# Kernel tuning notes

Hardware: AMD Instinct MI355X
Metric: run time of the kernel (lower is better)

The kernel has to match this reference:

```python
import jax, jax.numpy as jnp
import numpy as np

N, E = 20000, 320000
CS, CV = 64, 32          # scalar / vector multiplicities of node (= node_pre) irreps
AS_, AV, H = 16, 8, 4    # attn irreps scalar/vector muls, num_heads
NB = 16                  # num_basis
SQRT3 = 1.7320508075688772
SQRT2 = 1.4142135623730951
EPS = 1e-5

# dtp weight layout: [ss(CS), sv(CS), vs(CV), vv0(CV), vv1(CV)] -> numel = 2*CS+3*CV = 224

def _cg_tp(s, v, y0, y1, w_ss, w_sv, w_vs, w_vv0, w_vv1):
    """Depthwise CG tensor product for l<=1.
    s:(E,CS) v:(E,CV,3) y0:(E,) y1:(E,3); weights (E,C) or (C,).
    out scalars (E, CS+CV): 0e x 0e -> 0e, 1o x 1o -> 0e (dot/sqrt3)
    out vectors (E, CS+2*CV, 3): 0e x 1o -> 1o, 1o x 0e -> 1o, 1o x 1o -> 1o (cross/sqrt2)
    """
    out_s = jnp.concatenate([
        w_ss * s * y0[:, None],
        w_vv0 * (jnp.einsum('eci,ei->ec', v, y1) / SQRT3)], axis=-1)
    out_v = jnp.concatenate([
        (w_sv * s)[:, :, None] * y1[:, None, :],
        (w_vs * jnp.ones_like(v[..., 0]))[..., None] * v * y0[:, None, None],
        (w_vv1 * jnp.ones_like(v[..., 0]))[..., None] * (jnp.cross(v, y1[:, None, :]) / SQRT2)], axis=1)
    return out_s, out_v


def _equiv_layernorm(s, v, gamma_s, beta_s, gamma_v):
    mu = jnp.mean(s, axis=-1, keepdims=True)
    var = jnp.var(s, axis=-1, keepdims=True)
    s_n = (s - mu) * jax.lax.rsqrt(var + EPS) * gamma_s + beta_s
    rms = jnp.sqrt(jnp.mean(jnp.sum(v * v, axis=-1), axis=-1, keepdims=True) + EPS)
    v_n = v / rms[..., None] * gamma_v[None, :, None]
    return s_n, v_n


def setup_inputs() -> dict:
    key = jax.random.key(0)
    ks = jax.random.split(key, 26)
    def rn(k, shape, fan):
        return jax.random.normal(k, shape, jnp.float32) / np.sqrt(fan)
    D1S, D1V = CS + CV, CS + 2 * CV          # 96, 128 (dtp output muls)
    WN = 2 * CS + 3 * CV                     # 224 dtp weight numel
    inp = {
        'node': jax.random.normal(ks[0], (N, CS + 3 * CV), jnp.float32),
        'edge_index': jax.random.randint(ks[1], (2, E), 0, N, jnp.int64 if jax.config.jax_enable_x64 else jnp.int32),
        'rbf': jax.random.uniform(ks[2], (E, NB), jnp.float32),
        'rsh': jax.random.normal(ks[3], (E, 4), jnp.float32),
        'gamma_s': jnp.ones((CS,), jnp.float32),
        'beta_s': jnp.zeros((CS,), jnp.float32),
        'gamma_v': jnp.ones((CV,), jnp.float32),
        'Ws_src': rn(ks[4], (CS, CS), CS), 'Wv_src': rn(ks[5], (CV, CV), CV),
        'Ws_dst': rn(ks[6], (CS, CS), CS), 'Wv_dst': rn(ks[7], (CV, CV), CV),
        'W_rbf': rn(ks[8], (NB, WN), NB),
        'W_alpha': rn(ks[9], (D1S, H * AS_), D1S),
        'alpha_dot': rn(ks[10], (1, H, AS_), AS_),
        'Ws_val': rn(ks[11], (D1S, CS), D1S), 'Wv_val': rn(ks[12], (D1V, CV), D1V),
        'Wg': rn(ks[13], (CS, CV), CS),
        'w2_ss': rn(ks[14], (CS,), 1), 'w2_sv': rn(ks[15], (CS,), 1),
        'w2_vs': rn(ks[16], (CV,), 1), 'w2_vv0': rn(ks[17], (CV,), 1), 'w2_vv1': rn(ks[18], (CV,), 1),
        'Ws_vlin': rn(ks[19], (D1S, H * AS_), D1S), 'Wv_vlin': rn(ks[20], (D1V, H * AV), D1V),
        'Wps': rn(ks[21], (H * AS_, CS), H * AS_), 'Wpv': rn(ks[22], (H * AV, CV), H * AV),
    }
    return inp


def reference(node, rbf, rsh, gamma_s, beta_s, gamma_v, Ws_src, Wv_src, Ws_dst, Wv_dst,
              W_rbf, W_alpha, alpha_dot, Ws_val, Wv_val, Wg,
              w2_ss, w2_sv, w2_vs, w2_vv0, w2_vv1, Ws_vlin, Wv_vlin, Wps, Wpv, edge_index):
    n = node.shape[0]
    e = rsh.shape[0]
    s = node[:, :CS]
    v = node[:, CS:].reshape(n, CV, 3)
    # equivariant layer norm
    s_n, v_n = _equiv_layernorm(s, v, gamma_s, beta_s, gamma_v)
    # merge_src / merge_dst (irrep-wise o3.Linear)
    src, dst = edge_index[0], edge_index[1]
    msg_s = (s_n @ Ws_src)[src] + (s_n @ Ws_dst)[dst]                       # (E,CS)
    msg_v = jnp.einsum('ncx,cd->ndx', v_n, Wv_src)[src] + \
            jnp.einsum('ncx,cd->ndx', v_n, Wv_dst)[dst]                     # (E,CV,3)
    y0, y1 = rsh[:, 0], rsh[:, 1:4]
    # dtp1: per-edge weighted CG coupling, weights from rbf
    w1 = rbf @ W_rbf                                                        # (E,224)
    m1_s, m1_v = _cg_tp(msg_s, msg_v, y0, y1,
                        w1[:, :CS], w1[:, CS:2*CS], w1[:, 2*CS:2*CS+CV],
                        w1[:, 2*CS+CV:2*CS+2*CV], w1[:, 2*CS+2*CV:])        # (E,96) (E,128,3)
    # attention logits
    a = (m1_s @ W_alpha).reshape(e, H, AS_)
    a = jnp.where(a > 0, a, 0.2 * a)                                        # LeakyReLU(0.2)
    a = jnp.sum(a * alpha_dot, axis=-1, keepdims=True)                      # (E,H,1)
    # softmax over incoming edges of each destination node
    amax = jax.ops.segment_max(a, dst, num_segments=n)
    amax = jnp.where(jnp.isfinite(amax), amax, 0.0)
    ex = jnp.exp(a - amax[dst])
    den = jax.ops.segment_sum(ex, dst, num_segments=n)
    alpha = ex / (den[dst] + 1e-16)                                         # (E,H,1)
    # value path
    val_s = m1_s @ Ws_val                                                   # (E,CS)
    val_v = jnp.einsum('ecx,cd->edx', m1_v, Wv_val)                         # (E,CV,3)
    # gate: sigmoid on scalars, vectors gated by sigmoid of learned scalar gates
    val_v = val_v * jax.nn.sigmoid(val_s @ Wg)[..., None]
    val_s = jax.nn.sigmoid(val_s)
    # dtp2: shared internal weights
    m2_s, m2_v = _cg_tp(val_s, val_v, y0, y1, w2_ss, w2_sv, w2_vs, w2_vv0, w2_vv1)
    # value_lin -> (attn_irreps * num_heads), head-major layout
    hs = (m2_s @ Ws_vlin).reshape(e, H, AS_)
    hv = jnp.einsum('ecx,cd->edx', m2_v, Wv_vlin).reshape(e, H, AV, 3)
    h = jnp.concatenate([hs, hv.reshape(e, H, AV * 3)], axis=-1)            # (E,H,40)
    # attend + scatter-add to destination nodes
    agg = jax.ops.segment_sum(alpha * h, dst, num_segments=n)               # (N,H,40)
    agg_s = agg[:, :, :AS_].reshape(n, H * AS_)                             # (N,64)
    agg_v = agg[:, :, AS_:].reshape(n, H * AV, 3)                           # (N,32,3)
    out = node + jnp.concatenate([
        agg_s @ Wps,
        jnp.einsum('ncx,cd->ndx', agg_v, Wpv).reshape(n, CV * 3)], axis=-1)
    return out
```

## Files before the change

kernel.cpp:

```cpp
#include <hip/hip_runtime.h>
#include <hip/hip_bf16.h>
#include <cstddef>

typedef __hip_bfloat16 bf16;
typedef __bf16 bfv8 __attribute__((ext_vector_type(8)));
typedef __bf16 bfv4 __attribute__((ext_vector_type(4)));
typedef __bf16 bfv2 __attribute__((ext_vector_type(2)));
typedef float f4 __attribute__((ext_vector_type(4)));

#define EPSN 1e-5f
#define SQRT3_INV 0.57735026918962576f
#define SQRT2_INV 0.70710678118654752f

__device__ __forceinline__ float b2f(bf16 x) { return __bfloat162float(x); }

template<int BF> __device__ __forceinline__ float ldf(const void* p, size_t i) {
    if (BF) return __bfloat162float(((const bf16*)p)[i]);
    return ((const float*)p)[i];
}
__device__ __forceinline__ float ldr(const void* p, size_t i, int bfm) {
    return bfm ? __bfloat162float(((const bf16*)p)[i]) : ((const float*)p)[i];
}
template<int BF> __device__ __forceinline__ void stf(void* p, size_t i, float v) {
    if (BF) ((bf16*)p)[i] = __float2bfloat16(v);
    else    ((float*)p)[i] = v;
}

__device__ __forceinline__ float wave_sum64(float x) {
    #pragma unroll
    for (int m = 1; m < 64; m <<= 1) x += __shfl_xor(x, m, 64);
    return x;
}

__device__ __forceinline__ f4 mf(bfv8 a, bfv8 b, f4 c) {
    return __builtin_amdgcn_mfma_f32_16x16x32_bf16(a, b, c, 0, 0, 0);
}

__global__ __launch_bounds__(256) void k_sniff(const void* node, const void* eidx, int* flags)
{
    int t = threadIdx.x;
    __shared__ int cnt;
    __shared__ unsigned orr;
    if (t == 0) { cnt = 0; orr = 0u; }
    __syncthreads();
    unsigned w  = ((const unsigned*)node)[t];
    unsigned lo = w & 0xFFFFu;
    int e_lo = (int)((lo >> 7) & 0xFF);
    if (e_lo >= 96 && e_lo <= 140) atomicAdd(&cnt, 1);
    unsigned odd = ((const unsigned*)eidx)[2 * t + 1];
    atomicOr(&orr, odd);
    __syncthreads();
    if (t == 0) {
        flags[0] = (cnt >= 128) ? 1 : 0;
        flags[1] = (orr == 0u) ? 1 : 0;
    }
}

__global__ __launch_bounds__(256) void k_zero(float* p, int n)
{
    int i = blockIdx.x * 256 + threadIdx.x;
    if (i < n) p[i] = 0.f;
}

__global__ __launch_bounds__(256) void k_hist(const void* eidx, int* cnt,
                                              const int* flags, int E)
{
    int e = blockIdx.x * 256 + threadIdx.x;
    if (e >= E) return;
    int d = flags[1] ? (int)((const long long*)eidx)[(long long)E + e]
                     : ((const int*)eidx)[(size_t)E + e];
    atomicAdd(&cnt[d], 1);
}

__global__ __launch_bounds__(1024) void k_scan(int* cnt, int N)
{
    __shared__ int wsum[16];
    int t = threadIdx.x;
    int lane = t & 63, w = t >> 6;
    int chunk = (N + 1023) >> 10;
    int lo = t * chunk, hi = lo + chunk;
    if (hi > N) hi = N; if (lo > N) lo = N;
    int sum = 0;
    for (int i = lo; i < hi; ++i) sum += cnt[i];
    int x = sum;
    #pragma unroll
    for (int off = 1; off < 64; off <<= 1) {
        int y = __shfl_up(x, off, 64);
        if (lane >= off) x += y;
    }
    if (lane == 63) wsum[w] = x;
    __syncthreads();
    if (t < 64) {
        int v = (lane < 16) ? wsum[lane] : 0;
        #pragma unroll
        for (int off = 1; off < 16; off <<= 1) {
            int y = __shfl_up(v, off, 64);
            if (lane >= off) v += y;
        }
        if (lane < 16) wsum[lane] = v;
    }
    __syncthreads();
    int acc = x - sum + (w ? wsum[w - 1] : 0);
    for (int i = lo; i < hi; ++i) { int v = cnt[i]; cnt[i] = acc; acc += v; }
}

__global__ __launch_bounds__(256) void k_perm(const void* eidx, int* cnt, int* perm,
                                              const int* flags, int E)
{
    int e = blockIdx.x * 256 + threadIdx.x;
    if (e >= E) return;
    int d = flags[1] ? (int)((const long long*)eidx)[(long long)E + e]
                     : ((const int*)eidx)[(size_t)E + e];
    int pos = atomicAdd(&cnt[d], 1);
    perm[pos] = e;
}

template<int BF>
__device__ __forceinline__ void prep_impl(
    const void* Walpha, const void* Wsval, const void* Wsvlin,
    const void* Wvval, const void* Wvvlin, const void* Wg,
    const void* Wrbf, const void* adot,
    const void* w2ss, const void* w2sv, const void* w2vs,
    const void* w2vv0, const void* w2vv1,
    bf16* WalphaT, bf16* WsvalT, bf16* WsvlinT,
    bf16* WvvalT, bf16* WvvlinT, bf16* WgT,
    bf16* WrbfT, bf16* adotB, bf16* w2B)
{
    int t = threadIdx.x + blockIdx.x * 256;
    int T = gridDim.x * 256;
    for (int i = t; i < 96 * 64; i += T) {
        int c = i >> 6, n = i & 63;
        WalphaT[n * 96 + c] = __float2bfloat16(ldf<BF>(Walpha, i));
        WsvalT [n * 96 + c] = __float2bfloat16(ldf<BF>(Wsval,  i));
        WsvlinT[n * 96 + c] = __float2bfloat16(ldf<BF>(Wsvlin, i));
    }
    for (int i = t; i < 128 * 32; i += T) {
        int c = i >> 5, n = i & 31;
        WvvalT [n * 128 + c] = __float2bfloat16(ldf<BF>(Wvval,  i));
        WvvlinT[n * 128 + c] = __float2bfloat16(ldf<BF>(Wvvlin, i));
    }
    for (int i = t; i < 64 * 32; i += T) {
        int c = i >> 5, n = i & 31;
        WgT[n * 64 + c] = __float2bfloat16(ldf<BF>(Wg, i));
    }
    for (int i = t; i < 224 * 32; i += T) {
        int c = i >> 5, b = i & 31;
        WrbfT[i] = __float2bfloat16(b < 16 ? ldf<BF>(Wrbf, b * 224 + c) : 0.f);
    }
    if (t < 64) adotB[t] = __float2bfloat16(ldf<BF>(adot, t));
    if (t < 64) w2B[t]      = __float2bfloat16(ldf<BF>(w2ss, t));
    if (t < 64) w2B[64 + t] = __float2bfloat16(ldf<BF>(w2sv, t));
    if (t < 32) {
        w2B[128 + t] = __float2bfloat16(ldf<BF>(w2vs, t));
        w2B[160 + t] = __float2bfloat16(ldf<BF>(w2vv0, t));
        w2B[192 + t] = __float2bfloat16(ldf<BF>(w2vv1, t));
    }
}

__global__ __launch_bounds__(256) void k_prep(
    const void* Walpha, const void* Wsval, const void* Wsvlin,
    const void* Wvval, const void* Wvvlin, const void* Wg,
    const void* Wrbf, const void* adot,
    const void* w2ss, const void* w2sv, const void* w2vs,
    const void* w2vv0, const void* w2vv1,
    bf16* WalphaT, bf16* WsvalT, bf16* WsvlinT,
    bf16* WvvalT, bf16* WvvlinT, bf16* WgT,
    bf16* WrbfT, bf16* adotB, bf16* w2B, const int* flags)
{
    if (flags[0])
        prep_impl<1>(Walpha, Wsval, Wsvlin, Wvval, Wvvlin, Wg, Wrbf, adot,
                     w2ss, w2sv, w2vs, w2vv0, w2vv1,
                     WalphaT, WsvalT, WsvlinT, WvvalT, WvvlinT, WgT, WrbfT, adotB, w2B);
    else
        prep_impl<0>(Walpha, Wsval, Wsvlin, Wvval, Wvvlin, Wg, Wrbf, adot,
                     w2ss, w2sv, w2vs, w2vv0, w2vv1,
                     WalphaT, WsvalT, WsvlinT, WvvalT, WvvlinT, WgT, WrbfT, adotB, w2B);
}

template<int BF>
__device__ __forceinline__ void node_impl(
    const void* node, const void* gs, const void* bs, const void* gv,
    const void* Wss, const void* Wvs, const void* Wsd, const void* Wvd,
    bf16* ssrc, bf16* sdst, bf16* vsrcA, bf16* vdstA, bf16* vsrcB, bf16* vdstB,
    float* shs, float* shv, int n, int lane)
{
    size_t nb = (size_t)n * 160;

    float s  = ldf<BF>(node, nb + lane);
    float mu = wave_sum64(s) * (1.f / 64.f);
    float d  = s - mu;
    float var = wave_sum64(d * d) * (1.f / 64.f);
    float sn  = d * rsqrtf(var + EPSN) * ldf<BF>(gs, lane) + ldf<BF>(bs, lane);
    shs[lane] = sn;

    float v0 = 0.f, v1 = 0.f, v2 = 0.f, qq = 0.f;
    if (lane < 32) {
        v0 = ldf<BF>(node, nb + 64 + lane * 3 + 0);
        v1 = ldf<BF>(node, nb + 64 + lane * 3 + 1);
        v2 = ldf<BF>(node, nb + 64 + lane * 3 + 2);
        qq = v0 * v0 + v1 * v1 + v2 * v2;
    }
    float msq = wave_sum64(qq) * (1.f / 32.f);
    float inv = rsqrtf(msq + EPSN);
    if (lane < 32) {
        float g = ldf<BF>(gv, lane);
        shv[0 * 32 + lane] = v0 * inv * g;
        shv[1 * 32 + lane] = v1 * inv * g;
        shv[2 * 32 + lane] = v2 * inv * g;
    }

    float a1 = 0.f, a2 = 0.f;
    for (int c = 0; c < 64; ++c) {
        float sc = shs[c];
        a1 += sc * ldf<BF>(Wss, c * 64 + lane);
        a2 += sc * ldf<BF>(Wsd, c * 64 + lane);
    }
    {
        int cs = lane;
        int pos = (cs & 15) * 4 + (cs >> 4);
        ssrc[(size_t)n * 64 + pos] = __float2bfloat16(a1);
        sdst[(size_t)n * 64 + pos] = __float2bfloat16(a2);
    }

    {
        int x = lane >> 5, dd = lane & 31;
        float p1 = 0.f, p2 = 0.f;
        for (int c = 0; c < 32; ++c) {
            float vc = shv[x * 32 + c];
            p1 += vc * ldf<BF>(Wvs, c * 32 + dd);
            p2 += vc * ldf<BF>(Wvd, c * 32 + dd);
        }
        int mm = dd & 15, n2 = dd >> 4;
        int pos = mm * 4 + x * 2 + n2;
        vsrcA[(size_t)n * 64 + pos] = __float2bfloat16(p1);
        vdstA[(size_t)n * 64 + pos] = __float2bfloat16(p2);
    }
    if (lane < 32) {
        int dd = lane;
        float p1 = 0.f, p2 = 0.f;
        for (int c = 0; c < 32; ++c) {
            float vc = shv[2 * 32 + c];
            p1 += vc * ldf<BF>(Wvs, c * 32 + dd);
            p2 += vc * ldf<BF>(Wvd, c * 32 + dd);
        }
        int mm = dd & 15, n2 = dd >> 4;
        int pos = mm * 2 + n2;
        vsrcB[(size_t)n * 32 + pos] = __float2bfloat16(p1);
        vdstB[(size_t)n * 32 + pos] = __float2bfloat16(p2);
    }
}

__global__ __launch_bounds__(256) void k_node(
    const void* node, const void* gs, const void* bs, const void* gv,
    const void* Wss, const void* Wvs, const void* Wsd, const void* Wvd,
    bf16* ssrc, bf16* sdst, bf16* vsrcA, bf16* vdstA, bf16* vsrcB, bf16* vdstB,
    const int* flags, int N)
{
    __shared__ float shs[4][64];
    __shared__ float shv[4][96];
    int wv = threadIdx.x >> 6, lane = threadIdx.x & 63;
    int n = blockIdx.x * 4 + wv; if (n >= N) return;
    if (flags[0])
        node_impl<1>(node, gs, bs, gv, Wss, Wvs, Wsd, Wvd,
                     ssrc, sdst, vsrcA, vdstA, vsrcB, vdstB, shs[wv], shv[wv], n, lane);
    else
        node_impl<0>(node, gs, bs, gv, Wss, Wvs, Wsd, Wvd,
                     ssrc, sdst, vsrcA, vdstA, vsrcB, vdstB, shs[wv], shv[wv], n, lane);
}

static constexpr int SS  = 104;
static constexpr int A1S = 0;
static constexpr int SV  = 136;
static constexpr int P0  = 16 * SS;
static constexpr int P1  = P0 + 16 * SV;
static constexpr int VAL = 0;
static constexpr int SA  = 72;
static constexpr int HSZ = P1 + 16 * SV;

#define W_M1(X, PB) do { \
    constexpr int x_ = (X), x1_ = ((X)+1)%3, x2_ = ((X)+2)%3; \
    _Pragma("unroll") \
    for (int r = 0; r < 4; ++r) { \
        int e = q * 4 + r; \
        float4 yy = *(const float4*)&sY[wv][e][0]; \
        float y0 = yy.x; float yv[3] = {yy.y, yy.z, yy.w}; \
        _Pragma("unroll") \
        for (int nt = 0; nt < 4; ++nt) \
            H[(PB) + e * SV + nt * 16 + m] = (__bf16)(sv_[r][nt] * yv[x_]); \
        _Pragma("unroll") \
        for (int n2 = 0; n2 < 2; ++n2) { \
            int c = 64 + n2 * 16 + m; \
            H[(PB) + e * SV + c] = (__bf16)(qv_[r][n2][x_] * y0); \
            float cr = pv_[r][n2][x1_] * yv[x2_] - pv_[r][n2][x2_] * yv[x1_]; \
            H[(PB) + e * SV + 32 + c] = (__bf16)(cr * SQRT2_INV); \
        } \
    } \
} while (0)

#define W_M2(X, PB) do { \
    constexpr int x_ = (X), x1_ = ((X)+1)%3, x2_ = ((X)+2)%3; \
    _Pragma("unroll") \
    for (int r = 0; r < 4; ++r) { \
        int e = q * 4 + r; \
        float4 yy = *(const float4*)&sY[wv][e][0]; \
        float y0 = yy.x; float yv[3] = {yy.y, yy.z, yy.w}; \
        _Pragma("unroll") \
        for (int nt = 0; nt < 4; ++nt) \
            H[(PB) + e * SV + nt * 16 + m] = (__bf16)(c2sv[nt] * vals[nt][r] * yv[x_]); \
        _Pragma("unroll") \
        for (int n2 = 0; n2 < 2; ++n2) { \
            int c = 64 + n2 * 16 + m; \
            H[(PB) + e * SV + c] = (__bf16)(c2vs[n2] * vv[x_][n2][r] * y0); \
            float cr = vv[x1_][n2][r] * yv[x2_] - vv[x2_][n2][r] * yv[x1_]; \
            H[(PB) + e * SV + 32 + c] = (__bf16)(c2v1[n2] * cr * SQRT2_INV); \
        } \
    } \
} while (0)

#define MMA_H(PB, WH, O0, O1) do { \
    bfv8 fg_[4]; \
    _Pragma("unroll") \
    for (int kt = 0; kt < 4; ++kt) \
        fg_[kt] = *(const bfv8*)(H + (PB) + m * SV + kt * 32 + kq); \
    _Pragma("unroll") \
    for (int kt = 0; kt < 4; ++kt) { \
        O0 = mf(fg_[kt], WH[kt],     O0); \
        O1 = mf(fg_[kt], WH[4 + kt], O1); \
    } \
} while (0)

__global__ __launch_bounds__(256, 3) void k_edge(
    const void* __restrict__ eidx, const void* __restrict__ rbf, const void* __restrict__ rsh,
    const bf16* __restrict__ WalphaT, const bf16* __restrict__ WsvalT, const bf16* __restrict__ WsvlinT,
    const bf16* __restrict__ WvvalT, const bf16* __restrict__ WvvlinT, const bf16* __restrict__ WgT,
    const bf16* __restrict__ WrbfT, const bf16* __restrict__ adotB, const bf16* __restrict__ w2B,
    const bf16* __restrict__ ssrc, const bf16* __restrict__ sdst,
    const bf16* __restrict__ vsrcA, const bf16* __restrict__ vdstA,
    const bf16* __restrict__ vsrcB, const bf16* __restrict__ vdstB,
    const int* __restrict__ perm,
    float* __restrict__ den, float* __restrict__ agg,
    const int* __restrict__ flags, int E)
{
    const int bfm = flags[0];
    const int i64 = flags[1];

    __shared__ __align__(16) __bf16 sH[4][HSZ];
    __shared__ __align__(16) float sY[4][16][4];
    __shared__ int sSD[4][48];

    int wv = threadIdx.x >> 6, l = threadIdx.x & 63;
    int q = l >> 4, m = l & 15;
    const int kq = q * 8;

    int bid;
    {
        int nwg = gridDim.x, orig = blockIdx.x;
        int qq_ = nwg >> 3, rr_ = nwg & 7;
        int xcd = orig & 7, off = orig >> 3;
        bid = (xcd < rr_ ? xcd * (qq_ + 1) : rr_ * (qq_ + 1) + (xcd - rr_) * qq_) + off;
    }
    long long eb = ((long long)bid * 4 + wv) * 16;
    if (eb >= E) return;
    __bf16* H = &sH[wv][0];

    if (l < 16) {
        long long p = eb + l; if (p > (long long)E - 1) p = E - 1;
        sSD[wv][32 + l] = perm[p];
    }
    if (l < 32) {
        int pe = sSD[wv][32 + (l & 15)];
        long long off = (l < 16) ? (long long)pe : ((long long)E + pe);
        sSD[wv][l] = i64 ? (int)((const long long*)eidx)[off] : ((const int*)eidx)[off];
    }
    {
        int pe = sSD[wv][32 + (l >> 2)];
        sY[wv][l >> 2][l & 3] = ldr(rsh, (size_t)pe * 4 + (l & 3), bfm);
    }

    f4 w1f[14];
    {
        bfv8 arb;
        #pragma unroll
        for (int i = 0; i < 8; ++i) arb[i] = (__bf16)0.f;
        if (q < 2) {
            int pe = sSD[wv][32 + m];
            if (bfm) {
                arb = *(const bfv8*)((const __bf16*)rbf + (size_t)pe * 16 + kq);
            } else {
                const float* rp = (const float*)rbf + (size_t)pe * 16 + kq;
                #pragma unroll
                for (int i = 0; i < 8; ++i) arb[i] = (__bf16)rp[i];
            }
        }
        const __bf16* wb = (const __bf16*)WrbfT;
        #pragma unroll
        for (int nt = 0; nt < 14; ++nt) {
            bfv8 bb = *(const bfv8*)(wb + (size_t)(nt * 16 + m) * 32 + kq);
            f4 z = {0.f, 0.f, 0.f, 0.f};
            w1f[nt] = mf(arb, bb, z);
        }
    }

    bfv4 gs_[4], gd_[4], gvA[4], gwA[4];
    bfv2 gvB[4], gwB[4];
    #pragma unroll
    for (int r = 0; r < 4; ++r) {
        int e = q * 4 + r;
        int s = sSD[wv][e], d = sSD[wv][16 + e];
        gs_[r] = *(const bfv4*)((const __bf16*)ssrc  + (size_t)s * 64 + m * 4);
        gd_[r] = *(const bfv4*)((const __bf16*)sdst  + (size_t)d * 64 + m * 4);
        gvA[r] = *(const bfv4*)((const __bf16*)vsrcA + (size_t)s * 64 + m * 4);
        gwA[r] = *(const bfv4*)((const __bf16*)vdstA + (size_t)d * 64 + m * 4);
        gvB[r] = *(const bfv2*)((const __bf16*)vsrcB + (size_t)s * 32 + m * 2);
        gwB[r] = *(const bfv2*)((const __bf16*)vdstB + (size_t)d * 32 + m * 2);
    }
    float ms_[4][4], mv_[4][2][3];
    #pragma unroll
    for (int r = 0; r < 4; ++r) {
        #pragma unroll
        for (int nt = 0; nt < 4; ++nt)
            ms_[r][nt] = (float)gs_[r][nt] + (float)gd_[r][nt];
        #pragma unroll
        for (int n2 = 0; n2 < 2; ++n2) {
            mv_[r][n2][0] = (float)gvA[r][0 * 2 + n2] + (float)gwA[r][0 * 2 + n2];
            mv_[r][n2][1] = (float)gvA[r][1 * 2 + n2] + (float)gwA[r][1 * 2 + n2];
            mv_[r][n2][2] = (float)gvB[r][n2]         + (float)gwB[r][n2];
        }
    }

    float sv_[4][4], qv_[4][2][3], pv_[4][2][3];
    #pragma unroll
    for (int r = 0; r < 4; ++r) {
        int e = q * 4 + r;
        float4 yy = *(const float4*)&sY[wv][e][0];
        float y0 = yy.x, yx = yy.y, yh = yy.z, yz = yy.w;
        #pragma unroll
        for (int nt = 0; nt < 4; ++nt) {
            H[A1S + e * SS + nt * 16 + m] = (__bf16)(w1f[nt][r] * ms_[r][nt] * y0);
            sv_[r][nt] = w1f[4 + nt][r] * ms_[r][nt];
        }
        #pragma unroll
        for (int n2 = 0; n2 < 2; ++n2) {
            float dot = mv_[r][n2][0] * yx + mv_[r][n2][1] * yh + mv_[r][n2][2] * yz;
            H[A1S + e * SS + 64 + n2 * 16 + m] = (__bf16)(w1f[10 + n2][r] * dot * SQRT3_INV);
            #pragma unroll
            for (int x = 0; x < 3; ++x) {
                qv_[r][n2][x] = w1f[8 + n2][r]  * mv_[r][n2][x];
                pv_[r][n2][x] = w1f[12 + n2][r] * mv_[r][n2][x];
            }
        }
    }

    bfv8 a1s0 = *(const bfv8*)(H + A1S + m * SS + 0  + kq);
    bfv8 a1s1 = *(const bfv8*)(H + A1S + m * SS + 32 + kq);
    bfv8 a1s2 = *(const bfv8*)(H + A1S + m * SS + 64 + kq);

    f4 vals[4];
    #pragma unroll
    for (int nt = 0; nt < 4; ++nt) {
        const __bf16* bp = (const __bf16*)WsvalT + (size_t)(nt * 16 + m) * 96 + kq;
        f4 acc = {0.f, 0.f, 0.f, 0.f};
        acc = mf(a1s0, *(const bfv8*)(bp),      acc);
        acc = mf(a1s1, *(const bfv8*)(bp + 32), acc);
        acc = mf(a1s2, *(const bfv8*)(bp + 64), acc);
        vals[nt] = acc;
    }
    #pragma unroll
    for (int nt = 0; nt < 4; ++nt)
        #pragma unroll
        for (int r = 0; r < 4; ++r) {
            float v = vals[nt][r];
            H[VAL + (q * 4 + r) * SA + nt * 16 + m] = (__bf16)v;
            vals[nt][r] = 1.f / (1.f + __expf(-v));
        }

    f4 gate[2];
    {
        bfv8 av0 = *(const bfv8*)(H + VAL + m * SA + 0  + kq);
        bfv8 av1 = *(const bfv8*)(H + VAL + m * SA + 32 + kq);
        #pragma unroll
        for (int nt = 0; nt < 2; ++nt) {
            const __bf16* bp = (const __bf16*)WgT + (size_t)(nt * 16 + m) * 64 + kq;
            f4 acc = {0.f, 0.f, 0.f, 0.f};
            acc = mf(av0, *(const bfv8*)(bp),      acc);
            acc = mf(av1, *(const bfv8*)(bp + 32), acc);
            gate[nt] = acc;
        }
        #pragma unroll
        for (int nt = 0; nt < 2; ++nt)
            #pragma unroll
            for (int r = 0; r < 4; ++r)
                gate[nt][r] = 1.f / (1.f + __expf(-gate[nt][r]));
    }

    float ex_[4][4];
    #pragma unroll
    for (int nt = 0; nt < 4; ++nt) {
        const __bf16* bp = (const __bf16*)WalphaT + (size_t)(nt * 16 + m) * 96 + kq;
        f4 acc = {0.f, 0.f, 0.f, 0.f};
        acc = mf(a1s0, *(const bfv8*)(bp),      acc);
        acc = mf(a1s1, *(const bfv8*)(bp + 32), acc);
        acc = mf(a1s2, *(const bfv8*)(bp + 64), acc);
        float ad = b2f(adotB[nt * 16 + m]);
        #pragma unroll
        for (int r = 0; r < 4; ++r) {
            float tv = acc[r];
            tv = tv > 0.f ? tv : 0.2f * tv;
            tv *= ad;
            tv += __shfl_xor(tv, 1); tv += __shfl_xor(tv, 2);
            tv += __shfl_xor(tv, 4); tv += __shfl_xor(tv, 8);
            tv = fminf(fmaxf(tv, -60.f), 60.f);
            ex_[nt][r] = __expf(tv);
        }
    }

    f4 vv[3][2];
    #pragma unroll
    for (int x = 0; x < 3; ++x)
        #pragma unroll
        for (int nt = 0; nt < 2; ++nt)
            vv[x][nt] = (f4){0.f, 0.f, 0.f, 0.f};
    {
        bfv8 wh[8];
        #pragma unroll
        for (int nt = 0; nt < 2; ++nt)
            #pragma unroll
            for (int kt = 0; kt < 4; ++kt)
                wh[nt * 4 + kt] = *(const bfv8*)((const __bf16*)WvvalT
                                   + (size_t)(nt * 16 + m) * 128 + kt * 32 + kq);
        W_M1(0, P0);
        W_M1(1, P1);
        MMA_H(P0, wh, vv[0][0], vv[0][1]);
        W_M1(2, P0);
        MMA_H(P1, wh, vv[1][0], vv[1][1]);
        MMA_H(P0, wh, vv[2][0], vv[2][1]);
    }
    #pragma unroll
    for (int x = 0; x < 3; ++x)
        #pragma unroll
        for (int nt = 0; nt < 2; ++nt)
            #pragma unroll
            for (int r = 0; r < 4; ++r)
                vv[x][nt][r] *= gate[nt][r];

    float c2ss[4], c2sv[4];
    #pragma unroll
    for (int nt = 0; nt < 4; ++nt) {
        c2ss[nt] = b2f(w2B[nt * 16 + m]);
        c2sv[nt] = b2f(w2B[64 + nt * 16 + m]);
    }
    float c2vs[2], c2v0[2], c2v1[2];
    #pragma unroll
    for (int nt = 0; nt < 2; ++nt) {
        c2vs[nt] = b2f(w2B[128 + nt * 16 + m]);
        c2v0[nt] = b2f(w2B[160 + nt * 16 + m]);
        c2v1[nt] = b2f(w2B[192 + nt * 16 + m]);
    }
    #pragma unroll
    for (int r = 0; r < 4; ++r) {
        int e = q * 4 + r;
        float4 yy = *(const float4*)&sY[wv][e][0];
        float y0 = yy.x, yx = yy.y, yh = yy.z, yz = yy.w;
        #pragma unroll
        for (int nt = 0; nt < 4; ++nt)
            H[A1S + e * SS + nt * 16 + m] = (__bf16)(c2ss[nt] * vals[nt][r] * y0);
        #pragma unroll
        for (int n2 = 0; n2 < 2; ++n2) {
            float dotv = vv[0][n2][r] * yx + vv[1][n2][r] * yh + vv[2][n2][r] * yz;
            H[A1S + e * SS + 64 + n2 * 16 + m] = (__bf16)(c2v0[n2] * dotv * SQRT3_INV);
        }
    }
    f4 hs[4];
    {
        bfv8 a2s0 = *(const bfv8*)(H + A1S + m * SS + 0  + kq);
        bfv8 a2s1 = *(const bfv8*)(H + A1S + m * SS + 32 + kq);
        bfv8 a2s2 = *(const bfv8*)(H + A1S + m * SS + 64 + kq);
        #pragma unroll
        for (int nt = 0; nt < 4; ++nt) {
            const __bf16* bp = (const __bf16*)WsvlinT + (size_t)(nt * 16 + m) * 96 + kq;
            f4 acc = {0.f, 0.f, 0.f, 0.f};
            acc = mf(a2s0, *(const bfv8*)(bp),      acc);
            acc = mf(a2s1, *(const bfv8*)(bp + 32), acc);
            acc = mf(a2s2, *(const bfv8*)(bp + 64), acc);
            hs[nt] = acc;
        }
    }

    f4 hv[3][2];
    #pragma unroll
    for (int x = 0; x < 3; ++x)
        #pragma unroll
        for (int nt = 0; nt < 2; ++nt)
            hv[x][nt] = (f4){0.f, 0.f, 0.f, 0.f};
    {
        bfv8 wh[8];
        #pragma unroll
        for (int nt = 0; nt < 2; ++nt)
            #pragma unroll
            for (int kt = 0; kt < 4; ++kt)
                wh[nt * 4 + kt] = *(const bfv8*)((const __bf16*)WvvlinT
                                   + (size_t)(nt * 16 + m) * 128 + kt * 32 + kq);
        W_M2(0, P0);
        W_M2(1, P1);
        MMA_H(P0, wh, hv[0][0], hv[0][1]);
        W_M2(2, P0);
        MMA_H(P1, wh, hv[1][0], hv[1][1]);
        MMA_H(P0, wh, hv[2][0], hv[2][1]);
    }

    float* Hf = (float*)H;
    #pragma unroll
    for (int r = 0; r < 4; ++r) {
        int e = q * 4 + r;
        float* row = Hf + e * 168;
        #pragma unroll
        for (int nt = 0; nt < 4; ++nt)
            row[nt * 40 + m] = ex_[nt][r] * hs[nt][r];
        #pragma unroll
        for (int nt = 0; nt < 2; ++nt) {
            int c = nt * 16 + m;
            int hh = c >> 3, dd = c & 7;
            float exv = (m >= 8) ? ex_[2 * nt + 1][r] : ex_[2 * nt][r];
            float* vb = row + hh * 40 + 16 + dd * 3;
            vb[0] = exv * hv[0][nt][r];
            vb[1] = exv * hv[1][nt][r];
            vb[2] = exv * hv[2][nt][r];
        }
        if (m < 4) row[160 + m] = ex_[m][r];
    }
    int nval = (int)((E - eb) < 16 ? (E - eb) : 16);
    {
        int s = 0;
        while (s < nval) {
            int d = sSD[wv][16 + s];
            int t = s + 1;
            while (t < nval && sSD[wv][16 + t] == d) ++t;
            float s0 = 0.f, s1 = 0.f, s2 = 0.f;
            for (int e = s; e < t; ++e) {
                const float* row = Hf + e * 168;
                s0 += row[l];
                s1 += row[64 + l];
                if (l < 36) s2 += row[128 + l];
            }
            float* rowp = agg + (size_t)d * 160;
            unsafeAtomicAdd(rowp + l, s0);
            unsafeAtomicAdd(rowp + 64 + l, s1);
            if (l < 32)      unsafeAtomicAdd(rowp + 128 + l, s2);
            else if (l < 36) unsafeAtomicAdd(den + (size_t)d * 4 + (l - 32), s2);
            s = t;
        }
    }
}

template<int BF>
__device__ __forceinline__ void out_impl(
    const void* node, const float* den, const float* agg,
    const void* Wps, const void* Wpv, void* out,
    float* shs, float* shv, float* sinv, int n, int lane)
{
    if (lane < 4) sinv[lane] = 1.f / (den[(size_t)n * 4 + lane] + 1e-16f);
    for (int idx = lane; idx < 160; idx += 64) {
        int h = idx / 40, r = idx - h * 40;
        float val = agg[(size_t)n * 160 + idx] * sinv[h];
        if (r < 16) shs[h * 16 + r] = val;
        else { int rr = r - 16; int dd = rr / 3, x = rr - dd * 3; shv[x * 32 + h * 8 + dd] = val; }
    }

    float acc = ldf<BF>(node, (size_t)n * 160 + lane);
    for (int c = 0; c < 64; ++c) acc += shs[c] * ldf<BF>(Wps, c * 64 + lane);
    stf<BF>(out, (size_t)n * 160 + lane, acc);

    {
        int idx = lane; int dd = idx / 3, x = idx - dd * 3;
        float a = ldf<BF>(node, (size_t)n * 160 + 64 + idx);
        for (int c = 0; c < 32; ++c) a += shv[x * 32 + c] * ldf<BF>(Wpv, c * 32 + dd);
        stf<BF>(out, (size_t)n * 160 + 64 + idx, a);
    }
    if (lane < 32) {
        int idx = 64 + lane; int dd = idx / 3, x = idx - dd * 3;
        float a = ldf<BF>(node, (size_t)n * 160 + 64 + idx);
        for (int c = 0; c < 32; ++c) a += shv[x * 32 + c] * ldf<BF>(Wpv, c * 32 + dd);
        stf<BF>(out, (size_t)n * 160 + 64 + idx, a);
    }
}

__global__ __launch_bounds__(256) void k_out(
    const void* node, const float* den, const float* agg,
    const void* Wps, const void* Wpv, void* out,
    const int* flags, int N)
{
    __shared__ float shs[4][64];
    __shared__ float shv[4][96];
    __shared__ float sinv[4][4];
    int wv = threadIdx.x >> 6, lane = threadIdx.x & 63;
    int n = blockIdx.x * 4 + wv; if (n >= N) return;
    if (flags[0])
        out_impl<1>(node, den, agg, Wps, Wpv, out, shs[wv], shv[wv], sinv[wv], n, lane);
    else
        out_impl<0>(node, den, agg, Wps, Wpv, out, shs[wv], shv[wv], sinv[wv], n, lane);
}

extern "C" void kernel_launch(void* const* d_in, const int* in_sizes, int n_in,
                              void* d_out, int out_size, void* d_ws, size_t ws_size,
                              hipStream_t stream)
{
    const void* node   = d_in[0];
    const void* eidx   = d_in[1];
    const void* rbf    = d_in[2];
    const void* rsh    = d_in[3];
    const void* gs     = d_in[4];
    const void* bs     = d_in[5];
    const void* gv     = d_in[6];
    const void* Wss    = d_in[7];
    const void* Wvs    = d_in[8];
    const void* Wsd    = d_in[9];
    const void* Wvd    = d_in[10];
    const void* Wrbf   = d_in[11];
    const void* Walpha = d_in[12];
    const void* adot   = d_in[13];
    const void* Wsval  = d_in[14];
    const void* Wvval  = d_in[15];
    const void* Wg     = d_in[16];
    const void* w2ss   = d_in[17];
    const void* w2sv   = d_in[18];
    const void* w2vs   = d_in[19];
    const void* w2vv0  = d_in[20];
    const void* w2vv1  = d_in[21];
    const void* Wsvlin = d_in[22];
    const void* Wvvlin = d_in[23];
    const void* Wps    = d_in[24];
    const void* Wpv    = d_in[25];

    int N = in_sizes[0] / 160;
    int E = in_sizes[1] / 2;

    char* base = (char*)d_ws;
    int*  flags   = (int*)base;
    bf16* WalphaT = (bf16*)(base + 16);
    bf16* WsvalT  = WalphaT + 6144;
    bf16* WsvlinT = WsvalT  + 6144;
    bf16* WvvalT  = WsvlinT + 6144;
    bf16* WvvlinT = WvvalT  + 4096;
    bf16* WgT     = WvvlinT + 4096;
    bf16* WrbfT   = WgT     + 2048;
    bf16* adotB   = WrbfT   + 7168;
    bf16* w2B     = adotB   + 64;
    bf16* ssrc    = w2B     + 224;
    bf16* sdst    = ssrc  + (size_t)N * 64;
    bf16* vsrcA   = sdst  + (size_t)N * 64;
    bf16* vdstA   = vsrcA + (size_t)N * 64;
    bf16* vsrcB   = vdstA + (size_t)N * 64;
    bf16* vdstB   = vsrcB + (size_t)N * 32;
    float* den    = (float*)(vdstB + (size_t)N * 32);
    float* agg    = den + (size_t)N * 4;
    int*  cnt     = (int*)(agg + (size_t)N * 160);
    int*  perm    = cnt + N;

    k_sniff<<<1, 256, 0, stream>>>(node, eidx, flags);
    int zn = N * 165;
    k_zero<<<(zn + 255) / 256, 256, 0, stream>>>(den, zn);

    int nbe = (E + 255) / 256;
    k_hist<<<nbe, 256, 0, stream>>>(eidx, cnt, flags, E);
    k_scan<<<1, 1024, 0, stream>>>(cnt, N);
    k_perm<<<nbe, 256, 0, stream>>>(eidx, cnt, perm, flags, E);

    k_prep<<<16, 256, 0, stream>>>(Walpha, Wsval, Wsvlin, Wvval, Wvvlin, Wg, Wrbf, adot,
                                   w2ss, w2sv, w2vs, w2vv0, w2vv1,
                                   WalphaT, WsvalT, WsvlinT, WvvalT, WvvlinT, WgT, WrbfT,
                                   adotB, w2B, flags);

    int nbn = (N + 3) / 4;
    k_node<<<nbn, 256, 0, stream>>>(node, gs, bs, gv, Wss, Wvs, Wsd, Wvd,
                                    ssrc, sdst, vsrcA, vdstA, vsrcB, vdstB, flags, N);

    int nb = (E + 63) / 64;
    k_edge<<<nb, 256, 0, stream>>>(eidx, rbf, rsh,
                                   WalphaT, WsvalT, WsvlinT, WvvalT, WvvlinT, WgT, WrbfT,
                                   adotB, w2B, ssrc, sdst, vsrcA, vdstA, vsrcB, vdstB,
                                   perm, den, agg, flags, E);

    int nbo = (N + 3) / 4;
    k_out<<<nbo, 256, 0, stream>>>(node, den, agg, Wps, Wpv, d_out, flags, N);
}
```

Baseline: 468.6 us.

## Merge small launches and shrink edge kernel LDS staging buffers

The sniff and zero kernels become one launch, and the weight-prep blocks are appended to the node kernel grid, which removes two kernel launches. In the edge kernel, the second staging region P1 is dropped: the three vector-component MMA stages reuse one buffer in sequence, and the per-edge H rows are written and scattered in two halves of 8 edges. This cuts the LDS footprint so more waves can be resident, at the cost of serialising stages that could previously overlap and adding another pass over the scatter loop.

```diff
diff --git a/kernel.cpp b/kernel.cpp
--- a/kernel.cpp
+++ b/kernel.cpp
@@ -36,30 +36,29 @@
     return __builtin_amdgcn_mfma_f32_16x16x32_bf16(a, b, c, 0, 0, 0);
 }
 
-__global__ __launch_bounds__(256) void k_sniff(const void* node, const void* eidx, int* flags)
+__global__ __launch_bounds__(256) void k_sniff_zero(const void* node, const void* eidx,
+                                                    int* flags, float* zp, int zn)
 {
     int t = threadIdx.x;
-    __shared__ int cnt;
-    __shared__ unsigned orr;
-    if (t == 0) { cnt = 0; orr = 0u; }
-    __syncthreads();
-    unsigned w  = ((const unsigned*)node)[t];
-    unsigned lo = w & 0xFFFFu;
-    int e_lo = (int)((lo >> 7) & 0xFF);
-    if (e_lo >= 96 && e_lo <= 140) atomicAdd(&cnt, 1);
-    unsigned odd = ((const unsigned*)eidx)[2 * t + 1];
-    atomicOr(&orr, odd);
-    __syncthreads();
-    if (t == 0) {
-        flags[0] = (cnt >= 128) ? 1 : 0;
-        flags[1] = (orr == 0u) ? 1 : 0;
-    }
-}
-
-__global__ __launch_bounds__(256) void k_zero(float* p, int n)
-{
-    int i = blockIdx.x * 256 + threadIdx.x;
-    if (i < n) p[i] = 0.f;
+    if (blockIdx.x == 0) {
+        __shared__ int cnt;
+        __shared__ unsigned orr;
+        if (t == 0) { cnt = 0; orr = 0u; }
+        __syncthreads();
+        unsigned w  = ((const unsigned*)node)[t];
+        unsigned lo = w & 0xFFFFu;
+        int e_lo = (int)((lo >> 7) & 0xFF);
+        if (e_lo >= 96 && e_lo <= 140) atomicAdd(&cnt, 1);
+        unsigned odd = ((const unsigned*)eidx)[2 * t + 1];
+        atomicOr(&orr, odd);
+        __syncthreads();
+        if (t == 0) {
+            flags[0] = (cnt >= 128) ? 1 : 0;
+            flags[1] = (orr == 0u) ? 1 : 0;
+        }
+    }
+    int i = blockIdx.x * 256 + t;
+    if (i < zn) zp[i] = 0.f;
 }
 
 __global__ __launch_bounds__(256) void k_hist(const void* eidx, int* cnt,
@@ -116,7 +115,7 @@
 }
 
 template<int BF>
-__device__ __forceinline__ void prep_impl(
+__device__ __forceinline__ void prep_body(int t, int T,
     const void* Walpha, const void* Wsval, const void* Wsvlin,
     const void* Wvval, const void* Wvvlin, const void* Wg,
     const void* Wrbf, const void* adot,
@@ -126,8 +125,6 @@
     bf16* WvvalT, bf16* WvvlinT, bf16* WgT,
     bf16* WrbfT, bf16* adotB, bf16* w2B)
 {
-    int t = threadIdx.x + blockIdx.x * 256;
-    int T = gridDim.x * 256;
     for (int i = t; i < 96 * 64; i += T) {
         int c = i >> 6, n = i & 63;
         WalphaT[n * 96 + c] = __float2bfloat16(ldf<BF>(Walpha, i));
@@ -157,7 +154,83 @@
     }
 }
 
-__global__ __launch_bounds__(256) void k_prep(
+template<int BF>
+__device__ __forceinline__ void node_body(
+    const void* node, const void* gs, const void* bs, const void* gv,
+    const void* Wss, const void* Wvs, const void* Wsd, const void* Wvd,
+    bf16* ssrc, bf16* sdst, bf16* vsrcA, bf16* vdstA, bf16* vsrcB, bf16* vdstB,
+    float* shs, float* shv, int n, int lane)
+{
+    size_t nb = (size_t)n * 160;
+
+    float s  = ldf<BF>(node, nb + lane);
+    float mu = wave_sum64(s) * (1.f / 64.f);
+    float d  = s - mu;
+    float var = wave_sum64(d * d) * (1.f / 64.f);
+    float sn  = d * rsqrtf(var + EPSN) * ldf<BF>(gs, lane) + ldf<BF>(bs, lane);
+    shs[lane] = sn;
+
+    float v0 = 0.f, v1 = 0.f, v2 = 0.f, qq = 0.f;
+    if (lane < 32) {
+        v0 = ldf<BF>(node, nb + 64 + lane * 3 + 0);
+        v1 = ldf<BF>(node, nb + 64 + lane * 3 + 1);
+        v2 = ldf<BF>(node, nb + 64 + lane * 3 + 2);
+        qq = v0 * v0 + v1 * v1 + v2 * v2;
+    }
+    float msq = wave_sum64(qq) * (1.f / 32.f);
+    float inv = rsqrtf(msq + EPSN);
+    if (lane < 32) {
+        float g = ldf<BF>(gv, lane);
+        shv[0 * 32 + lane] = v0 * inv * g;
+        shv[1 * 32 + lane] = v1 * inv * g;
+        shv[2 * 32 + lane] = v2 * inv * g;
+    }
+
+    float a1 = 0.f, a2 = 0.f;
+    for (int c = 0; c < 64; ++c) {
+        float sc = shs[c];
+        a1 += sc * ldf<BF>(Wss, c * 64 + lane);
+        a2 += sc * ldf<BF>(Wsd, c * 64 + lane);
+    }
+    {
+        int cs = lane;
+        int pos = (cs & 15) * 4 + (cs >> 4);
+        ssrc[(size_t)n * 64 + pos] = __float2bfloat16(a1);
+        sdst[(size_t)n * 64 + pos] = __float2bfloat16(a2);
+    }
+
+    {
+        int x = lane >> 5, dd = lane & 31;
+        float p1 = 0.f, p2 = 0.f;
+        for (int c = 0; c < 32; ++c) {
+            float vc = shv[x * 32 + c];
+            p1 += vc * ldf<BF>(Wvs, c * 32 + dd);
+            p2 += vc * ldf<BF>(Wvd, c * 32 + dd);
+        }
+        int mm = dd & 15, n2 = dd >> 4;
+        int pos = mm * 4 + x * 2 + n2;
+        vsrcA[(size_t)n * 64 + pos] = __float2bfloat16(p1);
+        vdstA[(size_t)n * 64 + pos] = __float2bfloat16(p2);
+    }
+    if (lane < 32) {
+        int dd = lane;
+        float p1 = 0.f, p2 = 0.f;
+        for (int c = 0; c < 32; ++c) {
+            float vc = shv[2 * 32 + c];
+            p1 += vc * ldf<BF>(Wvs, c * 32 + dd);
+            p2 += vc * ldf<BF>(Wvd, c * 32 + dd);
+        }
+        int mm = dd & 15, n2 = dd >> 4;
+        int pos = mm * 2 + n2;
+        vsrcB[(size_t)n * 32 + pos] = __float2bfloat16(p1);
+        vdstB[(size_t)n * 32 + pos] = __float2bfloat16(p2);
+    }
+}
+
+__global__ __launch_bounds__(256) void k_node(
+    const void* node, const void* gs, const void* bs, const void* gv,
+    const void* Wss, const void* Wvs, const void* Wsd, const void* Wvd,
+    bf16* ssrc, bf16* sdst, bf16* vsrcA, bf16* vdstA, bf16* vsrcB, bf16* vdstB,
     const void* Walpha, const void* Wsval, const void* Wsvlin,
     const void* Wvval, const void* Wvvlin, const void* Wg,
     const void* Wrbf, const void* adot,
@@ -165,106 +238,31 @@
     const void* w2vv0, const void* w2vv1,
     bf16* WalphaT, bf16* WsvalT, bf16* WsvlinT,
     bf16* WvvalT, bf16* WvvlinT, bf16* WgT,
-    bf16* WrbfT, bf16* adotB, bf16* w2B, const int* flags)
-{
-    if (flags[0])
-        prep_impl<1>(Walpha, Wsval, Wsvlin, Wvval, Wvvlin, Wg, Wrbf, adot,
-                     w2ss, w2sv, w2vs, w2vv0, w2vv1,
-                     WalphaT, WsvalT, WsvlinT, WvvalT, WvvlinT, WgT, WrbfT, adotB, w2B);
-    else
-        prep_impl<0>(Walpha, Wsval, Wsvlin, Wvval, Wvvlin, Wg, Wrbf, adot,
-                     w2ss, w2sv, w2vs, w2vv0, w2vv1,
-                     WalphaT, WsvalT, WsvlinT, WvvalT, WvvlinT, WgT, WrbfT, adotB, w2B);
-}
-
-template<int BF>
-__device__ __forceinline__ void node_impl(
-    const void* node, const void* gs, const void* bs, const void* gv,
-    const void* Wss, const void* Wvs, const void* Wsd, const void* Wvd,
-    bf16* ssrc, bf16* sdst, bf16* vsrcA, bf16* vdstA, bf16* vsrcB, bf16* vdstB,
-    float* shs, float* shv, int n, int lane)
-{
-    size_t nb = (size_t)n * 160;
-
-    float s  = ldf<BF>(node, nb + lane);
-    float mu = wave_sum64(s) * (1.f / 64.f);
-    float d  = s - mu;
-    float var = wave_sum64(d * d) * (1.f / 64.f);
-    float sn  = d * rsqrtf(var + EPSN) * ldf<BF>(gs, lane) + ldf<BF>(bs, lane);
-    shs[lane] = sn;
-
-    float v0 = 0.f, v1 = 0.f, v2 = 0.f, qq = 0.f;
-    if (lane < 32) {
-        v0 = ldf<BF>(node, nb + 64 + lane * 3 + 0);
-        v1 = ldf<BF>(node, nb + 64 + lane * 3 + 1);
-        v2 = ldf<BF>(node, nb + 64 + lane * 3 + 2);
-        qq = v0 * v0 + v1 * v1 + v2 * v2;
-    }
-    float msq = wave_sum64(qq) * (1.f / 32.f);
-    float inv = rsqrtf(msq + EPSN);
-    if (lane < 32) {
-        float g = ldf<BF>(gv, lane);
-        shv[0 * 32 + lane] = v0 * inv * g;
-        shv[1 * 32 + lane] = v1 * inv * g;
-        shv[2 * 32 + lane] = v2 * inv * g;
-    }
-
-    float a1 = 0.f, a2 = 0.f;
-    for (int c = 0; c < 64; ++c) {
-        float sc = shs[c];
-        a1 += sc * ldf<BF>(Wss, c * 64 + lane);
-        a2 += sc * ldf<BF>(Wsd, c * 64 + lane);
-    }
-    {
-        int cs = lane;
-        int pos = (cs & 15) * 4 + (cs >> 4);
-        ssrc[(size_t)n * 64 + pos] = __float2bfloat16(a1);
-        sdst[(size_t)n * 64 + pos] = __float2bfloat16(a2);
-    }
-
-    {
-        int x = lane >> 5, dd = lane & 31;
-        float p1 = 0.f, p2 = 0.f;
-        for (int c = 0; c < 32; ++c) {
-            float vc = shv[x * 32 + c];
-            p1 += vc * ldf<BF>(Wvs, c * 32 + dd);
-            p2 += vc * ldf<BF>(Wvd, c * 32 + dd);
-        }
-        int mm = dd & 15, n2 = dd >> 4;
-        int pos = mm * 4 + x * 2 + n2;
-        vsrcA[(size_t)n * 64 + pos] = __float2bfloat16(p1);
-        vdstA[(size_t)n * 64 + pos] = __float2bfloat16(p2);
-    }
-    if (lane < 32) {
-        int dd = lane;
-        float p1 = 0.f, p2 = 0.f;
-        for (int c = 0; c < 32; ++c) {
-            float vc = shv[2 * 32 + c];
-            p1 += vc * ldf<BF>(Wvs, c * 32 + dd);
-            p2 += vc * ldf<BF>(Wvd, c * 32 + dd);
-        }
-        int mm = dd & 15, n2 = dd >> 4;
-        int pos = mm * 2 + n2;
-        vsrcB[(size_t)n * 32 + pos] = __float2bfloat16(p1);
-        vdstB[(size_t)n * 32 + pos] = __float2bfloat16(p2);
-    }
-}
-
-__global__ __launch_bounds__(256) void k_node(
-    const void* node, const void* gs, const void* bs, const void* gv,
-    const void* Wss, const void* Wvs, const void* Wsd, const void* Wvd,
-    bf16* ssrc, bf16* sdst, bf16* vsrcA, bf16* vdstA, bf16* vsrcB, bf16* vdstB,
-    const int* flags, int N)
-{
+    bf16* WrbfT, bf16* adotB, bf16* w2B,
+    const int* flags, int nbn, int N)
+{
+    if ((int)blockIdx.x >= nbn) {
+        int t = (blockIdx.x - nbn) * 256 + threadIdx.x;
+        int T = 16 * 256;
+        if (flags[0])
+            prep_body<1>(t, T, Walpha, Wsval, Wsvlin, Wvval, Wvvlin, Wg, Wrbf, adot,
+                         w2ss, w2sv, w2vs, w2vv0, w2vv1,
+                         WalphaT, WsvalT, WsvlinT, WvvalT, WvvlinT, WgT, WrbfT, adotB, w2B);
+        else
+            prep_body<0>(t, T, Walpha, Wsval, Wsvlin, Wvval, Wvvlin, Wg, Wrbf, adot,
+                         w2ss, w2sv, w2vs, w2vv0, w2vv1,
+                         WalphaT, WsvalT, WsvlinT, WvvalT, WvvlinT, WgT, WrbfT, adotB, w2B);
+        return;
+    }
     __shared__ float shs[4][64];
     __shared__ float shv[4][96];
     int wv = threadIdx.x >> 6, lane = threadIdx.x & 63;
     int n = blockIdx.x * 4 + wv; if (n >= N) return;
     if (flags[0])
-        node_impl<1>(node, gs, bs, gv, Wss, Wvs, Wsd, Wvd,
+        node_body<1>(node, gs, bs, gv, Wss, Wvs, Wsd, Wvd,
                      ssrc, sdst, vsrcA, vdstA, vsrcB, vdstB, shs[wv], shv[wv], n, lane);
     else
-        node_impl<0>(node, gs, bs, gv, Wss, Wvs, Wsd, Wvd,
+        node_body<0>(node, gs, bs, gv, Wss, Wvs, Wsd, Wvd,
                      ssrc, sdst, vsrcA, vdstA, vsrcB, vdstB, shs[wv], shv[wv], n, lane);
 }
 
@@ -272,10 +270,9 @@
 static constexpr int A1S = 0;
 static constexpr int SV  = 136;
 static constexpr int P0  = 16 * SS;
-static constexpr int P1  = P0 + 16 * SV;
 static constexpr int VAL = 0;
 static constexpr int SA  = 72;
-static constexpr int HSZ = P1 + 16 * SV;
+static constexpr int HSZ = P0 + 16 * SV;
 
 #define W_M1(X, PB) do { \
     constexpr int x_ = (X), x1_ = ((X)+1)%3, x2_ = ((X)+2)%3; \
@@ -529,10 +526,10 @@
                 wh[nt * 4 + kt] = *(const bfv8*)((const __bf16*)WvvalT
                                    + (size_t)(nt * 16 + m) * 128 + kt * 32 + kq);
         W_M1(0, P0);
-        W_M1(1, P1);
         MMA_H(P0, wh, vv[0][0], vv[0][1]);
+        W_M1(1, P0);
+        MMA_H(P0, wh, vv[1][0], vv[1][1]);
         W_M1(2, P0);
-        MMA_H(P1, wh, vv[1][0], vv[1][1]);
         MMA_H(P0, wh, vv[2][0], vv[2][1]);
     }
     #pragma unroll
@@ -601,53 +598,60 @@
                 wh[nt * 4 + kt] = *(const bfv8*)((const __bf16*)WvvlinT
                                    + (size_t)(nt * 16 + m) * 128 + kt * 32 + kq);
         W_M2(0, P0);
-        W_M2(1, P1);
         MMA_H(P0, wh, hv[0][0], hv[0][1]);
+        W_M2(1, P0);
+        MMA_H(P0, wh, hv[1][0], hv[1][1]);
         W_M2(2, P0);
-        MMA_H(P1, wh, hv[1][0], hv[1][1]);
         MMA_H(P0, wh, hv[2][0], hv[2][1]);
     }
 
-    float* Hf = (float*)H;
-    #pragma unroll
-    for (int r = 0; r < 4; ++r) {
-        int e = q * 4 + r;
-        float* row = Hf + e * 168;
-        #pragma unroll
-        for (int nt = 0; nt < 4; ++nt)
-            row[nt * 40 + m] = ex_[nt][r] * hs[nt][r];
-        #pragma unroll
-        for (int nt = 0; nt < 2; ++nt) {
-            int c = nt * 16 + m;
-            int hh = c >> 3, dd = c & 7;
-            float exv = (m >= 8) ? ex_[2 * nt + 1][r] : ex_[2 * nt][r];
-            float* vb = row + hh * 40 + 16 + dd * 3;
-            vb[0] = exv * hv[0][nt][r];
-            vb[1] = exv * hv[1][nt][r];
-            vb[2] = exv * hv[2][nt][r];
-        }
-        if (m < 4) row[160 + m] = ex_[m][r];
-    }
-    int nval = (int)((E - eb) < 16 ? (E - eb) : 16);
-    {
-        int s = 0;
-        while (s < nval) {
-            int d = sSD[wv][16 + s];
-            int t = s + 1;
-            while (t < nval && sSD[wv][16 + t] == d) ++t;
-            float s0 = 0.f, s1 = 0.f, s2 = 0.f;
-            for (int e = s; e < t; ++e) {
-                const float* row = Hf + e * 168;
-                s0 += row[l];
-                s1 += row[64 + l];
-                if (l < 36) s2 += row[128 + l];
+    {
+        float* Hf = (float*)H;
+        int nval = (int)((E - eb) < 16 ? (E - eb) : 16);
+        #pragma unroll
+        for (int half = 0; half < 2; ++half) {
+            if ((q >> 1) == half) {
+                #pragma unroll
+                for (int r = 0; r < 4; ++r) {
+                    int er = (q & 1) * 4 + r;
+                    float* row = Hf + er * 168;
+                    #pragma unroll
+                    for (int nt = 0; nt < 4; ++nt)
+                        row[nt * 40 + m] = ex_[nt][r] * hs[nt][r];
+                    #pragma unroll
+                    for (int nt = 0; nt < 2; ++nt) {
+                        int c = nt * 16 + m;
+                        int hh = c >> 3, dd = c & 7;
+                        float exv = (m >= 8) ? ex_[2 * nt + 1][r] : ex_[2 * nt][r];
+                        float* vb = row + hh * 40 + 16 + dd * 3;
+                        vb[0] = exv * hv[0][nt][r];
+                        vb[1] = exv * hv[1][nt][r];
+                        vb[2] = exv * hv[2][nt][r];
+                    }
+                    if (m < 4) row[160 + m] = ex_[m][r];
+                }
             }
-            float* rowp = agg + (size_t)d * 160;
-            unsafeAtomicAdd(rowp + l, s0);
-            unsafeAtomicAdd(rowp + 64 + l, s1);
-            if (l < 32)      unsafeAtomicAdd(rowp + 128 + l, s2);
-            else if (l < 36) unsafeAtomicAdd(den + (size_t)d * 4 + (l - 32), s2);
-            s = t;
+            int lo = half * 8;
+            int hi = nval < lo + 8 ? nval : lo + 8;
+            int s = lo;
+            while (s < hi) {
+                int d = sSD[wv][16 + s];
+                int t2 = s + 1;
+                while (t2 < hi && sSD[wv][16 + t2] == d) ++t2;
+                float s0 = 0.f, s1 = 0.f, s2 = 0.f;
+                for (int e = s; e < t2; ++e) {
+                    const float* row = Hf + (e - lo) * 168;
+                    s0 += row[l];
+                    s1 += row[64 + l];
+                    if (l < 36) s2 += row[128 + l];
+                }
+                float* rowp = agg + (size_t)d * 160;
+                unsafeAtomicAdd(rowp + l, s0);
+                unsafeAtomicAdd(rowp + 64 + l, s1);
+                if (l < 32)      unsafeAtomicAdd(rowp + 128 + l, s2);
+                else if (l < 36) unsafeAtomicAdd(den + (size_t)d * 4 + (l - 32), s2);
+                s = t2;
+            }
         }
     }
 }
@@ -756,23 +760,21 @@
     int*  cnt     = (int*)(agg + (size_t)N * 160);
     int*  perm    = cnt + N;
 
-    k_sniff<<<1, 256, 0, stream>>>(node, eidx, flags);
     int zn = N * 165;
-    k_zero<<<(zn + 255) / 256, 256, 0, stream>>>(den, zn);
+    k_sniff_zero<<<(zn + 255) / 256, 256, 0, stream>>>(node, eidx, flags, den, zn);
 
     int nbe = (E + 255) / 256;
     k_hist<<<nbe, 256, 0, stream>>>(eidx, cnt, flags, E);
     k_scan<<<1, 1024, 0, stream>>>(cnt, N);
     k_perm<<<nbe, 256, 0, stream>>>(eidx, cnt, perm, flags, E);
 
-    k_prep<<<16, 256, 0, stream>>>(Walpha, Wsval, Wsvlin, Wvval, Wvvlin, Wg, Wrbf, adot,
-                                   w2ss, w2sv, w2vs, w2vv0, w2vv1,
-                                   WalphaT, WsvalT, WsvlinT, WvvalT, WvvlinT, WgT, WrbfT,
-                                   adotB, w2B, flags);
-
     int nbn = (N + 3) / 4;
-    k_node<<<nbn, 256, 0, stream>>>(node, gs, bs, gv, Wss, Wvs, Wsd, Wvd,
-                                    ssrc, sdst, vsrcA, vdstA, vsrcB, vdstB, flags, N);
+    k_node<<<nbn + 16, 256, 0, stream>>>(node, gs, bs, gv, Wss, Wvs, Wsd, Wvd,
+                                         ssrc, sdst, vsrcA, vdstA, vsrcB, vdstB,
+                                         Walpha, Wsval, Wsvlin, Wvval, Wvvlin, Wg,
+                                         Wrbf, adot, w2ss, w2sv, w2vs, w2vv0, w2vv1,
+                                         WalphaT, WsvalT, WsvlinT, WvvalT, WvvlinT,
+                                         WgT, WrbfT, adotB, w2B, flags, nbn, N);
 
     int nb = (E + 63) / 64;
     k_edge<<<nb, 256, 0, stream>>>(eidx, rbf, rsh,
```

Measured after the change: 446.2 us. -4.8%, faster.
